# Optimization experiments

Hardware: AMD Instinct MI355X
Metric: run time of the kernel (lower is better)

## Reference

```python
import jax, jax.numpy as jnp
import numpy as np
from math import sqrt

D_MODEL = 768
N_HEADS = 12
D_K = 64
D_V = 64
LN_EPS = 1e-5
NEG = -1e9


def layer_norm(x, g, b):
    mu = jnp.mean(x, axis=-1, keepdims=True)
    var = jnp.mean((x - mu) ** 2, axis=-1, keepdims=True)
    return (x - mu) * jax.lax.rsqrt(var + LN_EPS) * g + b


def setup_inputs() -> dict:
    key = jax.random.key(0)
    ks = jax.random.split(key, 8)
    B, S = 4, 1024
    pro1 = jax.random.normal(ks[0], (B, S, D_MODEL), dtype=jnp.float32)
    pro2 = jax.random.normal(ks[1], (B, S, D_MODEL), dtype=jnp.float32)
    # attn_mask is [B, H, S2, S1]; transpose(2,3) masks scores [B,H,S1,S2]
    mask1_2 = jax.random.bernoulli(ks[2], 0.3, (B, N_HEADS, S, S))
    sc = 1.0 / np.sqrt(D_MODEL)
    W_Q = jax.random.normal(ks[3], (D_MODEL, D_K * N_HEADS), dtype=jnp.float32) * sc
    W_K = jax.random.normal(ks[4], (D_MODEL, D_K * N_HEADS), dtype=jnp.float32) * sc
    fc1 = jax.random.normal(ks[5], (D_V * N_HEADS, D_MODEL), dtype=jnp.float32) * sc
    g1 = jnp.ones((D_MODEL,), jnp.float32)
    b1 = jnp.zeros((D_MODEL,), jnp.float32)
    g2 = jnp.ones((D_MODEL,), jnp.float32)
    b2 = jnp.zeros((D_MODEL,), jnp.float32)
    return {"pro1": pro1, "pro2": pro2, "mask1_2": mask1_2,
            "W_Q": W_Q, "W_K": W_K, "fc1": fc1,
            "g1": g1, "b1": b1, "g2": g2, "b2": b2}


def reference(pro1, pro2, mask1_2, W_Q, W_K, fc1, g1, b1, g2, b2):
    B, S1, _ = pro1.shape
    S2 = pro2.shape[1]
    # project and split heads: [B, H, S, d_k]
    Q = (pro1 @ W_Q).reshape(B, S1, N_HEADS, D_K).transpose(0, 2, 1, 3)
    K = (pro2 @ W_K).reshape(B, S2, N_HEADS, D_K).transpose(0, 2, 1, 3)
    scores = jnp.einsum('bhsd,bhtd->bhst', Q, K) / sqrt(D_K)  # [B,H,S1,S2]
    mask = jnp.swapaxes(mask1_2, 2, 3)  # attn_mask.transpose(2,3)
    scores = jnp.where(mask, NEG, scores)
    attn1 = jax.nn.softmax(scores, axis=-1)                  # over S2
    attn2 = jax.nn.softmax(jnp.swapaxes(scores, -1, -2), axis=-1)  # over S1
    ctx1 = jnp.einsum('bhst,bhtd->bhsd', attn1, K)  # [B,H,S1,d_k]
    ctx2 = jnp.einsum('bhts,bhsd->bhtd', attn2, Q)  # [B,H,S2,d_k]
    c1 = ctx1.transpose(0, 2, 1, 3).reshape(B, S1, N_HEADS * D_V)
    c2 = ctx2.transpose(0, 2, 1, 3).reshape(B, S2, N_HEADS * D_V)
    # NOTE: original applies fc1 to BOTH branches (fc2 is dead code)
    o1 = layer_norm(c1 @ fc1, g1, b1)
    o2 = layer_norm(c2 @ fc1, g2, b2)
    return (o1, o2)
```

## Files before the change

### kernel.cpp

```cpp
#include <hip/hip_runtime.h>
#include <hip/hip_bf16.h>
#include <stdint.h>

#define S 1024
#define DMODEL 768
#define NH 12
#define DK 64
#define BB 4
#define BH 48
#define M4 4096

typedef __attribute__((ext_vector_type(8))) short bf16x8;
typedef __attribute__((ext_vector_type(4))) float f32x4;
typedef __attribute__((ext_vector_type(4))) _Float16 f16x4;
typedef __attribute__((ext_vector_type(8))) _Float16 f16x8;

static __device__ __forceinline__ unsigned short f2bf(float f) {
  unsigned int u = __float_as_uint(f);
  unsigned int r = u + 0x7FFFu + ((u >> 16) & 1u);
  return (unsigned short)(r >> 16);
}
static __device__ __forceinline__ bf16x8 ldfrag(const unsigned short* p) {
  uint4 q = *reinterpret_cast<const uint4*>(p);
  return __builtin_bit_cast(bf16x8, q);
}
static __device__ __forceinline__ f16x8 ldfragh(const unsigned short* p) {
  uint4 q = *reinterpret_cast<const uint4*>(p);
  return __builtin_bit_cast(f16x8, q);
}
static __device__ __forceinline__ unsigned short h2u(_Float16 h) {
  return __builtin_bit_cast(unsigned short, h);
}
static __device__ __forceinline__ void gl2lds16(const unsigned short* g, unsigned short* l) {
  __builtin_amdgcn_global_load_lds(
      (const __attribute__((address_space(1))) unsigned int*)g,
      (__attribute__((address_space(3))) unsigned int*)l, 16, 0, 0);
}

__global__ __launch_bounds__(256) void k_convert(const float* __restrict__ in,
                                                 unsigned short* __restrict__ out, int n4) {
  int i = blockIdx.x * 256 + threadIdx.x;
  if (i < n4) {
    float4 v = reinterpret_cast<const float4*>(in)[i];
    ushort4 o;
    o.x = f2bf(v.x); o.y = f2bf(v.y); o.z = f2bf(v.z); o.w = f2bf(v.w);
    reinterpret_cast<ushort4*>(out)[i] = o;
  }
}

__global__ __launch_bounds__(256) void k_transpose(const float* w0, const float* w1, const float* w2,
                                                   unsigned short* o0, unsigned short* o1, unsigned short* o2) {
  const float* in = blockIdx.z == 0 ? w0 : (blockIdx.z == 1 ? w1 : w2);
  unsigned short* out = blockIdx.z == 0 ? o0 : (blockIdx.z == 1 ? o1 : o2);
  __shared__ float tile[32][33];
  int n0 = blockIdx.x * 32, k0 = blockIdx.y * 32;
  int tid = threadIdx.x;
  int r = tid >> 3, c = (tid & 7) * 4;
  float4 v = *reinterpret_cast<const float4*>(in + (size_t)(k0 + r) * DMODEL + n0 + c);
  tile[r][c] = v.x; tile[r][c + 1] = v.y; tile[r][c + 2] = v.z; tile[r][c + 3] = v.w;
  __syncthreads();
  ushort4 o;
  o.x = f2bf(tile[c + 0][r]);
  o.y = f2bf(tile[c + 1][r]);
  o.z = f2bf(tile[c + 2][r]);
  o.w = f2bf(tile[c + 3][r]);
  *reinterpret_cast<ushort4*>(out + (size_t)(n0 + r) * DMODEL + k0 + c) = o;
}

__global__ __launch_bounds__(256) void k_pack(const int* __restrict__ mask,
                                              unsigned int* __restrict__ mp2) {
  int bh = blockIdx.y;
  int w = threadIdx.x >> 6, lane = threadIdx.x & 63;
  int tile = blockIdx.x * 4 + w;
  int ti = tile >> 4, tj = tile & 15;
  int t0 = ti * 64, s0 = tj * 64;
  const int* mb = mask + (size_t)bh * S * S;
  unsigned long long rowword = 0;
#pragma unroll 8
  for (int r = 0; r < 64; ++r) {
    int v = mb[(size_t)(t0 + r) * S + s0 + lane];
    unsigned long long b = __ballot(v != 0);
    if (lane == r) rowword = b;
  }
  unsigned int* p2 = mp2 + (size_t)bh * 32 * S;
  p2[((s0 >> 5) + 0) * S + t0 + lane] = (unsigned int)rowword;
  p2[((s0 >> 5) + 1) * S + t0 + lane] = (unsigned int)(rowword >> 32);
}

__global__ __launch_bounds__(256, 3) void k_gemm(
    int mode,
    const unsigned short* __restrict__ A0, const unsigned short* __restrict__ A1,
    const unsigned short* __restrict__ Bt0, const unsigned short* __restrict__ Bt1,
    unsigned short* __restrict__ oQ0, unsigned short* __restrict__ oQ1,
    unsigned short* __restrict__ oT0, unsigned short* __restrict__ oT1,
    float* __restrict__ oF0, float* __restrict__ oF1) {
  const unsigned short* A = blockIdx.z ? A1 : A0;
  const unsigned short* Bt = blockIdx.z ? Bt1 : Bt0;
  __shared__ __align__(16) unsigned short As[128 * 64];
  __shared__ __align__(16) unsigned short Bs[128 * 64];
  int tid = threadIdx.x;
  int m0 = blockIdx.x * 128, n0 = blockIdx.y * 128;
  int w = tid >> 6, lane = tid & 63, lane15 = lane & 15, quad = lane >> 4;
  int row0 = (w >> 1) * 64, col0 = (w & 1) * 64;
  f32x4 acc[4][4] = {};

  const unsigned short* gA[4];
  const unsigned short* gB[4];
  unsigned short* lA[4];
  unsigned short* lB[4];
  {
    int lr = lane >> 3;
    int ch = lane & 7;
#pragma unroll
    for (int i = 0; i < 4; ++i) {
      int r = w * 32 + i * 8 + lr;
      int cs = ((ch ^ (r & 7)) * 8);
      gA[i] = A + (size_t)(m0 + r) * DMODEL + cs;
      gB[i] = Bt + (size_t)(n0 + r) * DMODEL + cs;
      lA[i] = &As[(w * 32 + i * 8) * 64];
      lB[i] = &Bs[(w * 32 + i * 8) * 64];
    }
  }
  int l7 = lane15 & 7;
#pragma unroll
  for (int i = 0; i < 4; ++i) { gl2lds16(gA[i], lA[i]); gl2lds16(gB[i], lB[i]); }

  for (int kc = 0; kc < 12; ++kc) {
    __syncthreads();
#pragma unroll
    for (int ks = 0; ks < 2; ++ks) {
      int co = (((ks * 4 + quad) ^ l7) * 8);
      bf16x8 a[4], b[4];
#pragma unroll
      for (int i = 0; i < 4; ++i) a[i] = ldfrag(&As[(row0 + i * 16 + lane15) * 64 + co]);
#pragma unroll
      for (int j = 0; j < 4; ++j) b[j] = ldfrag(&Bs[(col0 + j * 16 + lane15) * 64 + co]);
#pragma unroll
      for (int i = 0; i < 4; ++i)
#pragma unroll
        for (int j = 0; j < 4; ++j)
          acc[i][j] = __builtin_amdgcn_mfma_f32_16x16x32_bf16(a[i], b[j], acc[i][j], 0, 0, 0);
    }
    __syncthreads();
    if (kc < 11) {
      int ko = (kc + 1) * 64;
#pragma unroll
      for (int i = 0; i < 4; ++i) { gl2lds16(gA[i] + ko, lA[i]); gl2lds16(gB[i] + ko, lB[i]); }
    }
  }

  if (mode == 0) {
    unsigned short* out = blockIdx.z ? oQ1 : oQ0;
    unsigned short* outT = blockIdx.z ? oT1 : oT0;
    f16x4 iden;
#pragma unroll
    for (int i = 0; i < 4; ++i) iden[i] = (_Float16)((quad * 4 + i) == lane15 ? 1.0f : 0.0f);
    f32x4 zero4 = {};
#pragma unroll
    for (int i = 0; i < 4; ++i)
#pragma unroll
      for (int j = 0; j < 4; ++j) {
        f16x4 cf;
#pragma unroll
        for (int reg = 0; reg < 4; ++reg) cf[reg] = (_Float16)acc[i][j][reg];
        f32x4 tq = __builtin_amdgcn_mfma_f32_16x16x16f16(cf, iden, zero4, 0, 0, 0);
        {
          int m = m0 + row0 + i * 16 + lane15;
          int n = n0 + col0 + j * 16 + quad * 4;
          int b = m >> 10, s = m & 1023, h = n >> 6, d = n & 63;
          ushort4 o;
          o.x = h2u((_Float16)tq[0]); o.y = h2u((_Float16)tq[1]);
          o.z = h2u((_Float16)tq[2]); o.w = h2u((_Float16)tq[3]);
          *reinterpret_cast<ushort4*>(&out[(((size_t)(b * NH + h)) * S + s) * DK + d]) = o;
        }
        {
          int n = n0 + col0 + j * 16 + lane15;
          int m = m0 + row0 + i * 16 + quad * 4;
          int b = m >> 10, s = m & 1023, h = n >> 6, d = n & 63;
          ushort4 o;
          o.x = h2u((_Float16)acc[i][j][0]); o.y = h2u((_Float16)acc[i][j][1]);
          o.z = h2u((_Float16)acc[i][j][2]); o.w = h2u((_Float16)acc[i][j][3]);
          *reinterpret_cast<ushort4*>(&outT[(((size_t)(b * NH + h)) * DK + d) * S + s]) = o;
        }
      }
  } else {
    float* out = blockIdx.z ? oF1 : oF0;
#pragma unroll
    for (int i = 0; i < 4; ++i)
#pragma unroll
      for (int j = 0; j < 4; ++j)
#pragma unroll
        for (int reg = 0; reg < 4; ++reg) {
          int m = m0 + row0 + i * 16 + quad * 4 + reg;
          int n = n0 + col0 + j * 16 + lane15;
          out[(size_t)m * DMODEL + n] = acc[i][j][reg];
        }
  }
}

__global__ __launch_bounds__(256, 3) void k_attn(
    const unsigned short* __restrict__ Qb, const unsigned short* __restrict__ Kb,
    const unsigned short* __restrict__ QT, const unsigned short* __restrict__ KT,
    const unsigned int* __restrict__ mp2,
    unsigned short* __restrict__ c1, unsigned short* __restrict__ c2) {
  int bh = blockIdx.y, path = blockIdx.z;
  int s0b = blockIdx.x * 128;
  const unsigned short* X = path ? Kb : Qb;
  const unsigned short* Y = path ? Qb : Kb;
  const unsigned short* YT = path ? QT : KT;
  unsigned short* outc = path ? c2 : c1;

  __shared__ __align__(16) unsigned short YS[64 * 72];
  __shared__ __align__(16) unsigned short YTS[64 * 72];
  __shared__ unsigned int MWS[256];

  const unsigned short* Xb = X + (size_t)bh * S * DK;
  const unsigned short* Yb = Y + (size_t)bh * S * DK;
  const unsigned short* YTb = YT + (size_t)bh * DK * S;
  const unsigned int* mbg = mp2 + (size_t)bh * 32 * S;

  int tid = threadIdx.x;
  int w = tid >> 6, lane = tid & 63, lane15 = lane & 15, quad = lane >> 4;
  int s0w = s0b + w * 32;

  f16x8 xf[2][2];
#pragma unroll
  for (int rg = 0; rg < 2; ++rg) {
    xf[rg][0] = ldfragh(Xb + (size_t)(s0w + rg * 16 + lane15) * DK + quad * 8);
    xf[rg][1] = ldfragh(Xb + (size_t)(s0w + rg * 16 + lane15) * DK + 32 + quad * 8);
  }

  int sr4 = tid >> 2, sc4 = (tid & 3) * 16;
  const unsigned short* gY = Yb + (size_t)sr4 * DK + sc4;
  const unsigned short* gYT = YTb + (size_t)sr4 * S + sc4;
  uint4 y0 = *reinterpret_cast<const uint4*>(gY);
  uint4 y1 = *reinterpret_cast<const uint4*>(gY + 8);
  uint4 t0 = *reinterpret_cast<const uint4*>(gYT);
  uint4 t1 = *reinterpret_cast<const uint4*>(gYT + 8);
  int mws_idx = (path == 0) ? ((tid & 63) * 4 + (tid >> 6)) : ((tid & 127) * 2 + (tid >> 7));
  unsigned int mwv = (path == 0)
      ? mbg[((size_t)((s0b >> 5) + (tid >> 6))) * S + (tid & 63)]
      : mbg[((size_t)(tid >> 7)) * S + s0b + (tid & 127)];

  f32x4 outa[2][4] = {};
  float lsum[2] = {0.f, 0.f};

  for (int jc = 0; jc < 16; ++jc) {
    __syncthreads();
    *reinterpret_cast<uint4*>(&YS[sr4 * 72 + sc4]) = y0;
    *reinterpret_cast<uint4*>(&YS[sr4 * 72 + sc4 + 8]) = y1;
    *reinterpret_cast<uint4*>(&YTS[sr4 * 72 + sc4]) = t0;
    *reinterpret_cast<uint4*>(&YTS[sr4 * 72 + sc4 + 8]) = t1;
    MWS[mws_idx] = mwv;
    {
      int jn = (jc + 1 < 16) ? (jc + 1) * 64 : jc * 64;
      y0 = *reinterpret_cast<const uint4*>(gY + (size_t)jn * DK);
      y1 = *reinterpret_cast<const uint4*>(gY + (size_t)jn * DK + 8);
      t0 = *reinterpret_cast<const uint4*>(gYT + jn);
      t1 = *reinterpret_cast<const uint4*>(gYT + jn + 8);
      mwv = (path == 0)
          ? mbg[((size_t)((s0b >> 5) + (tid >> 6))) * S + jn + (tid & 63)]
          : mbg[((size_t)((jn >> 5) + (tid >> 7))) * S + s0b + (tid & 127)];
    }
    __syncthreads();

    f32x4 scv[4][2];
#pragma unroll
    for (int st = 0; st < 4; ++st) {
      f16x8 a0 = ldfragh(&YS[(st * 16 + lane15) * 72 + quad * 8]);
      f16x8 a1 = ldfragh(&YS[(st * 16 + lane15) * 72 + 32 + quad * 8]);
#pragma unroll
      for (int rg = 0; rg < 2; ++rg) {
        f32x4 v = {};
        v = __builtin_amdgcn_mfma_f32_16x16x32_f16(a0, xf[rg][0], v, 0, 0, 0);
        v = __builtin_amdgcn_mfma_f32_16x16x32_f16(a1, xf[rg][1], v, 0, 0, 0);
        scv[st][rg] = v;
      }
    }
    f16x4 pfa[4][2];
    if (path == 0) {
#pragma unroll
      for (int st = 0; st < 4; ++st)
#pragma unroll
        for (int reg = 0; reg < 4; ++reg) {
          unsigned int wdv = MWS[(st * 16 + quad * 4 + reg) * 4 + w];
#pragma unroll
          for (int rg = 0; rg < 2; ++rg) {
            float e = __expf(scv[st][rg][reg] * 0.125f);
            float p = ((wdv >> (unsigned)(rg * 16 + lane15)) & 1u) ? 0.f : e;
            lsum[rg] += p;
            pfa[st][rg][reg] = (_Float16)p;
          }
        }
    } else {
#pragma unroll
      for (int rg = 0; rg < 2; ++rg) {
        unsigned int wv0 = MWS[(w * 32 + rg * 16 + lane15) * 2 + 0];
        unsigned int wv1 = MWS[(w * 32 + rg * 16 + lane15) * 2 + 1];
#pragma unroll
        for (int st = 0; st < 4; ++st) {
          unsigned int wdv = (st < 2) ? wv0 : wv1;
#pragma unroll
          for (int reg = 0; reg < 4; ++reg) {
            unsigned int sh = (unsigned)((st & 1) * 16 + quad * 4 + reg);
            float e = __expf(scv[st][rg][reg] * 0.125f);
            float p = ((wdv >> sh) & 1u) ? 0.f : e;
            lsum[rg] += p;
            pfa[st][rg][reg] = (_Float16)p;
          }
        }
      }
    }
#pragma unroll
    for (int st = 0; st < 4; ++st)
#pragma unroll
      for (int dsub = 0; dsub < 4; ++dsub) {
        uint2 q = *reinterpret_cast<const uint2*>(&YTS[(dsub * 16 + lane15) * 72 + st * 16 + quad * 4]);
        f16x4 yb = __builtin_bit_cast(f16x4, q);
#pragma unroll
        for (int rg = 0; rg < 2; ++rg)
          outa[rg][dsub] = __builtin_amdgcn_mfma_f32_16x16x16f16(pfa[st][rg], yb, outa[rg][dsub], 0, 0, 0);
      }
  }

#pragma unroll
  for (int rg = 0; rg < 2; ++rg) {
    lsum[rg] += __shfl_xor(lsum[rg], 16);
    lsum[rg] += __shfl_xor(lsum[rg], 32);
  }
  float rinv[2][4];
#pragma unroll
  for (int rg = 0; rg < 2; ++rg)
#pragma unroll
    for (int reg = 0; reg < 4; ++reg)
      rinv[rg][reg] = 1.0f / __shfl(lsum[rg], quad * 4 + reg);

  int b = bh / NH, h = bh % NH;
#pragma unroll
  for (int rg = 0; rg < 2; ++rg)
#pragma unroll
    for (int dsub = 0; dsub < 4; ++dsub)
#pragma unroll
      for (int reg = 0; reg < 4; ++reg) {
        float v = outa[rg][dsub][reg] * rinv[rg][reg];
        int srow = s0w + rg * 16 + quad * 4 + reg;
        size_t idx = ((size_t)(b * S) + srow) * DMODEL + h * DK + dsub * 16 + lane15;
        outc[idx] = f2bf(v);
      }
}

__global__ __launch_bounds__(256) void k_ln(const float* __restrict__ f1, const float* __restrict__ f2,
                                            const float* __restrict__ g1, const float* __restrict__ b1,
                                            const float* __restrict__ g2, const float* __restrict__ b2,
                                            float* __restrict__ out) {
  int rowg = blockIdx.x;
  int sel = rowg >> 12;
  int row = rowg & 4095;
  const float* in = sel ? f2 : f1;
  const float* g = sel ? g2 : g1;
  const float* be = sel ? b2 : b1;
  int tid = threadIdx.x;
  const float* p = in + (size_t)row * DMODEL;
  float x0 = p[tid], x1 = p[tid + 256], x2 = p[tid + 512];
  float s = x0 + x1 + x2;
  float ss = x0 * x0 + x1 * x1 + x2 * x2;
#pragma unroll
  for (int m = 1; m < 64; m <<= 1) { s += __shfl_xor(s, m); ss += __shfl_xor(ss, m); }
  __shared__ float ps[4], pss[4];
  int w = tid >> 6;
  if ((tid & 63) == 0) { ps[w] = s; pss[w] = ss; }
  __syncthreads();
  s = ps[0] + ps[1] + ps[2] + ps[3];
  ss = pss[0] + pss[1] + pss[2] + pss[3];
  float mu = s * (1.0f / 768.0f);
  float var = ss * (1.0f / 768.0f) - mu * mu;
  float rstd = rsqrtf(var + 1e-5f);
  float* o = out + ((size_t)sel * M4 + row) * DMODEL;
  o[tid] = (x0 - mu) * rstd * g[tid] + be[tid];
  o[tid + 256] = (x1 - mu) * rstd * g[tid + 256] + be[tid + 256];
  o[tid + 512] = (x2 - mu) * rstd * g[tid + 512] + be[tid + 512];
}

extern "C" void kernel_launch(void* const* d_in, const int* in_sizes, int n_in,
                              void* d_out, int out_size, void* d_ws, size_t ws_size,
                              hipStream_t stream) {
  const float* pro1 = (const float*)d_in[0];
  const float* pro2 = (const float*)d_in[1];
  const int* mask = (const int*)d_in[2];
  const float* WQ = (const float*)d_in[3];
  const float* WK = (const float*)d_in[4];
  const float* FC1 = (const float*)d_in[5];
  const float* g1 = (const float*)d_in[6];
  const float* b1 = (const float*)d_in[7];
  const float* g2 = (const float*)d_in[8];
  const float* b2 = (const float*)d_in[9];
  float* out = (float*)d_out;
  char* ws = (char*)d_ws;

  unsigned short* pro1b = (unsigned short*)(ws + 0);
  unsigned short* pro2b = (unsigned short*)(ws + 6291456);
  float* f1 = (float*)(ws + 0);
  unsigned short* wqt = (unsigned short*)(ws + 12582912);
  unsigned short* wkt = (unsigned short*)(ws + 13762560);
  unsigned short* fc1t = (unsigned short*)(ws + 14942208);
  unsigned short* Qb = (unsigned short*)(ws + 16121856);
  unsigned short* Kb = (unsigned short*)(ws + 22413312);
  unsigned short* QT = (unsigned short*)(ws + 28704768);
  unsigned short* KT = (unsigned short*)(ws + 34996224);
  unsigned int* mp2 = (unsigned int*)(ws + 41287680);
  float* f2 = (float*)(ws + 47579136);
  unsigned short* c1 = (unsigned short*)(ws + 60162048);
  unsigned short* c2 = (unsigned short*)(ws + 66453504);

  k_convert<<<3072, 256, 0, stream>>>(pro1, pro1b, 786432);
  k_convert<<<3072, 256, 0, stream>>>(pro2, pro2b, 786432);
  k_transpose<<<dim3(24, 24, 3), 256, 0, stream>>>(WQ, WK, FC1, wqt, wkt, fc1t);
  k_pack<<<dim3(64, BH), 256, 0, stream>>>(mask, mp2);
  k_gemm<<<dim3(32, 6, 2), 256, 0, stream>>>(0, pro1b, pro2b, wqt, wkt,
                                             Qb, Kb, QT, KT, nullptr, nullptr);
  k_attn<<<dim3(8, BH, 2), 256, 0, stream>>>(Qb, Kb, QT, KT, mp2, c1, c2);
  k_gemm<<<dim3(32, 6, 2), 256, 0, stream>>>(1, c1, c2, fc1t, fc1t,
                                             nullptr, nullptr, nullptr, nullptr, f1, f2);
  k_ln<<<8192, 256, 0, stream>>>(f1, f2, g1, b1, g2, b2, out);
}
```

Measured before the change: 418.8 us.

## Vectorize mask packing, double-buffer attention LDS, XCD-aware grid, fp16 intermediate

New measurement: 416.6 us. No clear change (-0.5%).

```diff
diff --git a/kernel.cpp b/kernel.cpp
--- a/kernel.cpp
+++ b/kernel.cpp
@@ -31,14 +31,25 @@
 static __device__ __forceinline__ unsigned short h2u(_Float16 h) {
   return __builtin_bit_cast(unsigned short, h);
 }
+static __device__ __forceinline__ f16x4 pack4(const float* p) {
+  auto lo = __builtin_amdgcn_cvt_pkrtz(p[0], p[1]);
+  auto hi = __builtin_amdgcn_cvt_pkrtz(p[2], p[3]);
+  uint2 u;
+  u.x = __builtin_bit_cast(unsigned int, lo);
+  u.y = __builtin_bit_cast(unsigned int, hi);
+  return __builtin_bit_cast(f16x4, u);
+}
 static __device__ __forceinline__ void gl2lds16(const unsigned short* g, unsigned short* l) {
   __builtin_amdgcn_global_load_lds(
       (const __attribute__((address_space(1))) unsigned int*)g,
       (__attribute__((address_space(3))) unsigned int*)l, 16, 0, 0);
 }
 
-__global__ __launch_bounds__(256) void k_convert(const float* __restrict__ in,
-                                                 unsigned short* __restrict__ out, int n4) {
+__global__ __launch_bounds__(256) void k_convert(const float* __restrict__ i0, const float* __restrict__ i1,
+                                                 unsigned short* __restrict__ o0, unsigned short* __restrict__ o1,
+                                                 int n4) {
+  const float* in = blockIdx.y ? i1 : i0;
+  unsigned short* out = blockIdx.y ? o1 : o0;
   int i = blockIdx.x * 256 + threadIdx.x;
   if (i < n4) {
     float4 v = reinterpret_cast<const float4*>(in)[i];
@@ -72,19 +83,24 @@
   int bh = blockIdx.y;
   int w = threadIdx.x >> 6, lane = threadIdx.x & 63;
   int tile = blockIdx.x * 4 + w;
-  int ti = tile >> 4, tj = tile & 15;
-  int t0 = ti * 64, s0 = tj * 64;
-  const int* mb = mask + (size_t)bh * S * S;
-  unsigned long long rowword = 0;
+  int rowg = tile >> 2, colg = tile & 3;
+  int t0 = rowg * 64;
+  const int* mb = mask + (size_t)bh * S * S + colg * 256;
+  unsigned long long b0 = 0, b1 = 0, b2 = 0, b3 = 0;
 #pragma unroll 8
   for (int r = 0; r < 64; ++r) {
-    int v = mb[(size_t)(t0 + r) * S + s0 + lane];
-    unsigned long long b = __ballot(v != 0);
-    if (lane == r) rowword = b;
-  }
-  unsigned int* p2 = mp2 + (size_t)bh * 32 * S;
-  p2[((s0 >> 5) + 0) * S + t0 + lane] = (unsigned int)rowword;
-  p2[((s0 >> 5) + 1) * S + t0 + lane] = (unsigned int)(rowword >> 32);
+    int4 v = *reinterpret_cast<const int4*>(mb + (size_t)(t0 + r) * S + lane * 4);
+    unsigned long long c0 = __ballot(v.x != 0);
+    unsigned long long c1 = __ballot(v.y != 0);
+    unsigned long long c2 = __ballot(v.z != 0);
+    unsigned long long c3 = __ballot(v.w != 0);
+    if (lane == r) { b0 = c0; b1 = c1; b2 = c2; b3 = c3; }
+  }
+  unsigned int* p2 = mp2 + (size_t)bh * 32 * S + (size_t)(colg * 8) * S + t0 + lane;
+  p2[(size_t)0 * S] = (unsigned)b0;  p2[(size_t)1 * S] = (unsigned)(b0 >> 32);
+  p2[(size_t)2 * S] = (unsigned)b1;  p2[(size_t)3 * S] = (unsigned)(b1 >> 32);
+  p2[(size_t)4 * S] = (unsigned)b2;  p2[(size_t)5 * S] = (unsigned)(b2 >> 32);
+  p2[(size_t)6 * S] = (unsigned)b3;  p2[(size_t)7 * S] = (unsigned)(b3 >> 32);
 }
 
 __global__ __launch_bounds__(256, 3) void k_gemm(
@@ -93,7 +109,7 @@
     const unsigned short* __restrict__ Bt0, const unsigned short* __restrict__ Bt1,
     unsigned short* __restrict__ oQ0, unsigned short* __restrict__ oQ1,
     unsigned short* __restrict__ oT0, unsigned short* __restrict__ oT1,
-    float* __restrict__ oF0, float* __restrict__ oF1) {
+    unsigned short* __restrict__ oH0, unsigned short* __restrict__ oH1) {
   const unsigned short* A = blockIdx.z ? A1 : A0;
   const unsigned short* Bt = blockIdx.z ? Bt1 : Bt0;
   __shared__ __align__(16) unsigned short As[128 * 64];
@@ -184,7 +200,7 @@
         }
       }
   } else {
-    float* out = blockIdx.z ? oF1 : oF0;
+    unsigned short* outh = blockIdx.z ? oH1 : oH0;
 #pragma unroll
     for (int i = 0; i < 4; ++i)
 #pragma unroll
@@ -193,7 +209,7 @@
         for (int reg = 0; reg < 4; ++reg) {
           int m = m0 + row0 + i * 16 + quad * 4 + reg;
           int n = n0 + col0 + j * 16 + lane15;
-          out[(size_t)m * DMODEL + n] = acc[i][j][reg];
+          outh[(size_t)m * DMODEL + n] = h2u((_Float16)acc[i][j][reg]);
         }
   }
 }
@@ -203,16 +219,22 @@
     const unsigned short* __restrict__ QT, const unsigned short* __restrict__ KT,
     const unsigned int* __restrict__ mp2,
     unsigned short* __restrict__ c1, unsigned short* __restrict__ c2) {
-  int bh = blockIdx.y, path = blockIdx.z;
-  int s0b = blockIdx.x * 128;
+  int lin = blockIdx.x;
+  int xcd = lin & 7, idx = lin >> 3;
+  int grp = xcd * 12 + (idx >> 3);
+  int sb = idx & 7;
+  int path = grp >= 48 ? 1 : 0;
+  int bh = grp - path * 48;
+  int s0b = sb * 128;
+
   const unsigned short* X = path ? Kb : Qb;
   const unsigned short* Y = path ? Qb : Kb;
   const unsigned short* YT = path ? QT : KT;
   unsigned short* outc = path ? c2 : c1;
 
-  __shared__ __align__(16) unsigned short YS[64 * 72];
-  __shared__ __align__(16) unsigned short YTS[64 * 72];
-  __shared__ unsigned int MWS[256];
+  __shared__ __align__(16) unsigned short YS[2][64 * 72];
+  __shared__ __align__(16) unsigned short YTS[2][64 * 72];
+  __shared__ __align__(16) unsigned int MWS[2][512];
 
   const unsigned short* Xb = X + (size_t)bh * S * DK;
   const unsigned short* Yb = Y + (size_t)bh * S * DK;
@@ -222,6 +244,8 @@
   int tid = threadIdx.x;
   int w = tid >> 6, lane = tid & 63, lane15 = lane & 15, quad = lane >> 4;
   int s0w = s0b + w * 32;
+  int ck = lane15 & 3;
+  int sh0 = w * 8 + (lane15 >> 2);
 
   f16x8 xf[2][2];
 #pragma unroll
@@ -237,38 +261,56 @@
   uint4 y1 = *reinterpret_cast<const uint4*>(gY + 8);
   uint4 t0 = *reinterpret_cast<const uint4*>(gYT);
   uint4 t1 = *reinterpret_cast<const uint4*>(gYT + 8);
-  int mws_idx = (path == 0) ? ((tid & 63) * 4 + (tid >> 6)) : ((tid & 127) * 2 + (tid >> 7));
-  unsigned int mwv = (path == 0)
-      ? mbg[((size_t)((s0b >> 5) + (tid >> 6))) * S + (tid & 63)]
-      : mbg[((size_t)(tid >> 7)) * S + s0b + (tid & 127)];
+
+  int mj = tid >> 2;
+  int p0wi = (sb >> 1) * 8 + (tid & 3) * 2 + (sb & 1);
+  int tl = tid >> 1;
+  int k0 = (tid & 1) * 2, k1 = k0 + 1;
+  unsigned mwv0, mwv1 = 0;
+  if (path == 0) {
+    mwv0 = mbg[(size_t)p0wi * S + mj];
+  } else {
+    mwv0 = mbg[(size_t)(k0 * 2) * S + s0b + tl];
+    mwv1 = mbg[(size_t)(k1 * 2) * S + s0b + tl];
+  }
 
   f32x4 outa[2][4] = {};
   float lsum[2] = {0.f, 0.f};
 
   for (int jc = 0; jc < 16; ++jc) {
-    __syncthreads();
-    *reinterpret_cast<uint4*>(&YS[sr4 * 72 + sc4]) = y0;
-    *reinterpret_cast<uint4*>(&YS[sr4 * 72 + sc4 + 8]) = y1;
-    *reinterpret_cast<uint4*>(&YTS[sr4 * 72 + sc4]) = t0;
-    *reinterpret_cast<uint4*>(&YTS[sr4 * 72 + sc4 + 8]) = t1;
-    MWS[mws_idx] = mwv;
+    int buf = jc & 1;
+    *reinterpret_cast<uint4*>(&YS[buf][sr4 * 72 + sc4]) = y0;
+    *reinterpret_cast<uint4*>(&YS[buf][sr4 * 72 + sc4 + 8]) = y1;
+    *reinterpret_cast<uint4*>(&YTS[buf][sr4 * 72 + sc4]) = t0;
+    *reinterpret_cast<uint4*>(&YTS[buf][sr4 * 72 + sc4 + 8]) = t1;
+    if (path == 0) {
+      MWS[buf][tid] = mwv0;
+    } else {
+      uint2 mw; mw.x = mwv0; mw.y = mwv1;
+      *reinterpret_cast<uint2*>(&MWS[buf][tid * 2]) = mw;
+    }
     {
-      int jn = (jc + 1 < 16) ? (jc + 1) * 64 : jc * 64;
+      int jcn = (jc + 1 < 16) ? jc + 1 : jc;
+      int jn = jcn * 64;
       y0 = *reinterpret_cast<const uint4*>(gY + (size_t)jn * DK);
       y1 = *reinterpret_cast<const uint4*>(gY + (size_t)jn * DK + 8);
       t0 = *reinterpret_cast<const uint4*>(gYT + jn);
       t1 = *reinterpret_cast<const uint4*>(gYT + jn + 8);
-      mwv = (path == 0)
-          ? mbg[((size_t)((s0b >> 5) + (tid >> 6))) * S + jn + (tid & 63)]
-          : mbg[((size_t)((jn >> 5) + (tid >> 7))) * S + s0b + (tid & 127)];
+      if (path == 0) {
+        mwv0 = mbg[(size_t)p0wi * S + jn + mj];
+      } else {
+        size_t wb = (size_t)((jcn >> 2) * 8 + ((jcn >> 1) & 1)) * S + s0b + tl;
+        mwv0 = mbg[wb + (size_t)(k0 * 2) * S];
+        mwv1 = mbg[wb + (size_t)(k1 * 2) * S];
+      }
     }
     __syncthreads();
 
     f32x4 scv[4][2];
 #pragma unroll
     for (int st = 0; st < 4; ++st) {
-      f16x8 a0 = ldfragh(&YS[(st * 16 + lane15) * 72 + quad * 8]);
-      f16x8 a1 = ldfragh(&YS[(st * 16 + lane15) * 72 + 32 + quad * 8]);
+      f16x8 a0 = ldfragh(&YS[buf][(st * 16 + lane15) * 72 + quad * 8]);
+      f16x8 a1 = ldfragh(&YS[buf][(st * 16 + lane15) * 72 + 32 + quad * 8]);
 #pragma unroll
       for (int rg = 0; rg < 2; ++rg) {
         f32x4 v = {};
@@ -280,34 +322,40 @@
     f16x4 pfa[4][2];
     if (path == 0) {
 #pragma unroll
-      for (int st = 0; st < 4; ++st)
+      for (int st = 0; st < 4; ++st) {
+        float pv[2][4];
 #pragma unroll
         for (int reg = 0; reg < 4; ++reg) {
-          unsigned int wdv = MWS[(st * 16 + quad * 4 + reg) * 4 + w];
+          unsigned wdv = MWS[buf][(st * 16 + quad * 4 + reg) * 4 + ck];
 #pragma unroll
           for (int rg = 0; rg < 2; ++rg) {
             float e = __expf(scv[st][rg][reg] * 0.125f);
-            float p = ((wdv >> (unsigned)(rg * 16 + lane15)) & 1u) ? 0.f : e;
+            float p = ((wdv >> (unsigned)(sh0 + rg * 4)) & 1u) ? 0.f : e;
             lsum[rg] += p;
-            pfa[st][rg][reg] = (_Float16)p;
+            pv[rg][reg] = p;
           }
         }
+        pfa[st][0] = pack4(pv[0]);
+        pfa[st][1] = pack4(pv[1]);
+      }
     } else {
 #pragma unroll
       for (int rg = 0; rg < 2; ++rg) {
-        unsigned int wv0 = MWS[(w * 32 + rg * 16 + lane15) * 2 + 0];
-        unsigned int wv1 = MWS[(w * 32 + rg * 16 + lane15) * 2 + 1];
+        int bidx = (w * 32 + rg * 16 + lane15) * 4;
+        uint4 wq = *reinterpret_cast<const uint4*>(&MWS[buf][bidx]);
+        unsigned wd4[4] = {wq.x, wq.y, wq.z, wq.w};
 #pragma unroll
         for (int st = 0; st < 4; ++st) {
-          unsigned int wdv = (st < 2) ? wv0 : wv1;
+          float pv[4];
+          unsigned shb = (unsigned)((jc & 1) * 16 + st * 4 + quad);
 #pragma unroll
           for (int reg = 0; reg < 4; ++reg) {
-            unsigned int sh = (unsigned)((st & 1) * 16 + quad * 4 + reg);
             float e = __expf(scv[st][rg][reg] * 0.125f);
-            float p = ((wdv >> sh) & 1u) ? 0.f : e;
+            float p = ((wd4[reg] >> shb) & 1u) ? 0.f : e;
             lsum[rg] += p;
-            pfa[st][rg][reg] = (_Float16)p;
+            pv[reg] = p;
           }
+          pfa[st][rg] = pack4(pv);
         }
       }
     }
@@ -315,7 +363,7 @@
     for (int st = 0; st < 4; ++st)
 #pragma unroll
       for (int dsub = 0; dsub < 4; ++dsub) {
-        uint2 q = *reinterpret_cast<const uint2*>(&YTS[(dsub * 16 + lane15) * 72 + st * 16 + quad * 4]);
+        uint2 q = *reinterpret_cast<const uint2*>(&YTS[buf][(dsub * 16 + lane15) * 72 + st * 16 + quad * 4]);
         f16x4 yb = __builtin_bit_cast(f16x4, q);
 #pragma unroll
         for (int rg = 0; rg < 2; ++rg)
@@ -344,24 +392,27 @@
       for (int reg = 0; reg < 4; ++reg) {
         float v = outa[rg][dsub][reg] * rinv[rg][reg];
         int srow = s0w + rg * 16 + quad * 4 + reg;
-        size_t idx = ((size_t)(b * S) + srow) * DMODEL + h * DK + dsub * 16 + lane15;
-        outc[idx] = f2bf(v);
-      }
-}
-
-__global__ __launch_bounds__(256) void k_ln(const float* __restrict__ f1, const float* __restrict__ f2,
+        size_t idxo = ((size_t)(b * S) + srow) * DMODEL + h * DK + dsub * 16 + lane15;
+        outc[idxo] = f2bf(v);
+      }
+}
+
+__global__ __launch_bounds__(256) void k_ln(const unsigned short* __restrict__ f1,
+                                            const unsigned short* __restrict__ f2,
                                             const float* __restrict__ g1, const float* __restrict__ b1,
                                             const float* __restrict__ g2, const float* __restrict__ b2,
                                             float* __restrict__ out) {
   int rowg = blockIdx.x;
   int sel = rowg >> 12;
   int row = rowg & 4095;
-  const float* in = sel ? f2 : f1;
+  const unsigned short* in = sel ? f2 : f1;
   const float* g = sel ? g2 : g1;
   const float* be = sel ? b2 : b1;
   int tid = threadIdx.x;
-  const float* p = in + (size_t)row * DMODEL;
-  float x0 = p[tid], x1 = p[tid + 256], x2 = p[tid + 512];
+  const unsigned short* p = in + (size_t)row * DMODEL;
+  float x0 = (float)__builtin_bit_cast(_Float16, p[tid]);
+  float x1 = (float)__builtin_bit_cast(_Float16, p[tid + 256]);
+  float x2 = (float)__builtin_bit_cast(_Float16, p[tid + 512]);
   float s = x0 + x1 + x2;
   float ss = x0 * x0 + x1 * x1 + x2 * x2;
 #pragma unroll
@@ -399,7 +450,7 @@
 
   unsigned short* pro1b = (unsigned short*)(ws + 0);
   unsigned short* pro2b = (unsigned short*)(ws + 6291456);
-  float* f1 = (float*)(ws + 0);
+  unsigned short* f1h = (unsigned short*)(ws + 0);
   unsigned short* wqt = (unsigned short*)(ws + 12582912);
   unsigned short* wkt = (unsigned short*)(ws + 13762560);
   unsigned short* fc1t = (unsigned short*)(ws + 14942208);
@@ -408,18 +459,17 @@
   unsigned short* QT = (unsigned short*)(ws + 28704768);
   unsigned short* KT = (unsigned short*)(ws + 34996224);
   unsigned int* mp2 = (unsigned int*)(ws + 41287680);
-  float* f2 = (float*)(ws + 47579136);
+  unsigned short* f2h = (unsigned short*)(ws + 47579136);
   unsigned short* c1 = (unsigned short*)(ws + 60162048);
   unsigned short* c2 = (unsigned short*)(ws + 66453504);
 
-  k_convert<<<3072, 256, 0, stream>>>(pro1, pro1b, 786432);
-  k_convert<<<3072, 256, 0, stream>>>(pro2, pro2b, 786432);
+  k_convert<<<dim3(3072, 2), 256, 0, stream>>>(pro1, pro2, pro1b, pro2b, 786432);
   k_transpose<<<dim3(24, 24, 3), 256, 0, stream>>>(WQ, WK, FC1, wqt, wkt, fc1t);
-  k_pack<<<dim3(64, BH), 256, 0, stream>>>(mask, mp2);
+  k_pack<<<dim3(16, BH), 256, 0, stream>>>(mask, mp2);
   k_gemm<<<dim3(32, 6, 2), 256, 0, stream>>>(0, pro1b, pro2b, wqt, wkt,
                                              Qb, Kb, QT, KT, nullptr, nullptr);
-  k_attn<<<dim3(8, BH, 2), 256, 0, stream>>>(Qb, Kb, QT, KT, mp2, c1, c2);
+  k_attn<<<dim3(768), 256, 0, stream>>>(Qb, Kb, QT, KT, mp2, c1, c2);
   k_gemm<<<dim3(32, 6, 2), 256, 0, stream>>>(1, c1, c2, fc1t, fc1t,
-                                             nullptr, nullptr, nullptr, nullptr, f1, f2);
-  k_ln<<<8192, 256, 0, stream>>>(f1, f2, g1, b1, g2, b2, out);
-}
+                                             nullptr, nullptr, nullptr, nullptr, f1h, f2h);
+  k_ln<<<8192, 256, 0, stream>>>(f1h, f2h, g1, b1, g2, b2, out);
+}
```
